# Kernel optimization log

Measured on AMD Instinct MI355X. Metric: run time of the kernel, lower is better.

## Reference

```python
import jax, jax.numpy as jnp
import numpy as np

N, E = 8000, 64000
DNE, DED, DXPD = 128, 128, 64
H, LMAX = 8, 2
S = 1 + 2 * LMAX            # 5 coefficient slots
CD = S * DNE                # coeff_dim = 640
DH = DNE // H               # head dim = 16
CH = CD // H                # coeff head = 80


def _lin(k, din, dout):
    # xavier-ish init for a [din, dout] weight used as x @ W
    return (jax.random.normal(k, (din, dout), jnp.float32) / np.sqrt(din)).astype(jnp.float32)


def _mlp(x, W1, b1, W2, b2):
    # Linear -> SiLU -> (Dropout p, eval) -> Linear
    return jax.nn.silu(x @ W1 + b1) @ W2 + b2


def _seg_sum(x, idx, n):
    return jax.ops.segment_sum(x, idx, num_segments=n)


def _rej(x, r):
    # vector_rejection: remove component of x [E,m,d] parallel to r [E,m]
    r3 = r[:, :, None]
    return x - jnp.sum(x * r3, axis=1, keepdims=True) * r3


def setup_inputs() -> dict:
    key = jax.random.key(0)
    ks = jax.random.split(key, 40)
    inp = {
        "h":  jax.random.normal(ks[0], (N, DNE), jnp.float32),
        "t":  jax.random.normal(ks[1], (E, DED), jnp.float32),
        "X1": jax.random.normal(ks[2], (N, 3, DNE), jnp.float32),
        "X2": jax.random.normal(ks[3], (N, 5, DNE), jnp.float32),
        "r1": jax.random.normal(ks[4], (E, 3), jnp.float32),
        "r2": jax.random.normal(ks[5], (E, 5), jnp.float32),
        "c":  jax.random.uniform(ks[6], (E, 1), jnp.float32),
        "edge": jax.random.randint(ks[7], (E, 2), 0, N, jnp.int32),
    }
    # GATA params
    inp["Wq"], inp["bq"] = _lin(ks[8], DNE, DNE), jnp.zeros((DNE,), jnp.float32)
    inp["Wk"], inp["bk"] = _lin(ks[9], DNE, DNE), jnp.zeros((DNE,), jnp.float32)
    inp["Wre"], inp["bre"] = _lin(ks[10], DED, DNE), jnp.zeros((DNE,), jnp.float32)
    inp["Wv1"], inp["bv1"] = _lin(ks[11], DNE, DNE), jnp.zeros((DNE,), jnp.float32)
    inp["Wv2"], inp["bv2"] = _lin(ks[12], DNE, CD), jnp.zeros((CD,), jnp.float32)
    inp["Wrs"], inp["brs"] = _lin(ks[13], DED, CD), jnp.zeros((CD,), jnp.float32)
    inp["Ws1"], inp["bs1"] = _lin(ks[14], DNE, DNE), jnp.zeros((DNE,), jnp.float32)
    inp["Ws2"], inp["bs2"] = _lin(ks[15], DNE, CD), jnp.zeros((CD,), jnp.float32)
    # HTR params
    inp["Wvq"] = _lin(ks[16], DNE, DXPD)
    inp["Wvk1"] = _lin(ks[17], DNE, DXPD)
    inp["Wvk2"] = _lin(ks[18], DNE, DXPD)
    inp["Ww1"], inp["bw1"] = _lin(ks[19], DXPD, DXPD), jnp.zeros((DXPD,), jnp.float32)
    inp["Ww2"], inp["bw2"] = _lin(ks[20], DXPD, DED), jnp.zeros((DED,), jnp.float32)
    inp["Wt1"], inp["bt1"] = _lin(ks[21], DED, DED), jnp.zeros((DED,), jnp.float32)
    inp["Wt2"], inp["bt2"] = _lin(ks[22], DED, DED), jnp.zeros((DED,), jnp.float32)
    return inp


def reference(h, t, X1, X2, r1, r2, c, edge,
              Wq, bq, Wk, bk, Wre, bre, Wv1, bv1, Wv2, bv2,
              Wrs, brs, Ws1, bs1, Ws2, bs2,
              Wvq, Wvk1, Wvk2, Ww1, bw1, Ww2, bw2, Wt1, bt1, Wt2, bt2):
    i, j = edge[:, 0], edge[:, 1]
    # multi-head attention logits over edges
    q = (h[i] @ Wq + bq).reshape(E, H, DH)
    k = (h[j] @ Wk + bk).reshape(E, H, DH)
    geom = jax.nn.silu(t @ Wre + bre).reshape(E, H, DH)
    alpha = jnp.sum(q * (k * geom), axis=-1)                       # [E,H]
    # segment softmax over destination node i
    mx = jnp.full((N, H), -jnp.inf, jnp.float32).at[i].max(alpha)
    mx = jnp.maximum(mx, -1e9)
    ex = jnp.exp(alpha - mx[i])
    den = jnp.maximum(_seg_sum(ex, i, N), 1e-12)
    attn = ex / den[i]
    deg = jnp.zeros((N,), jnp.float32).at[i].add(1.0)              # bincount
    attn = attn * (jnp.sqrt(deg[i]) / np.sqrt(DNE))[:, None]       # [E,H]
    # values + spatial branch
    v = _mlp(h[j], Wv1, bv1, Wv2, bv2).reshape(E, H, CH)
    sea = attn[:, :, None] * v
    tp = (t @ Wrs + brs).reshape(E, H, CH)
    s = _mlp(h[j], Ws1, bs1, Ws2, bs2).reshape(E, H, CH)
    spatial = tp * s * c[:, None, :]
    coeff = (sea + spatial).reshape(E, S, DNE)
    # scalar update
    h_out = h + _seg_sum(coeff[:, 0, :], i, N)
    # steerable updates (l = 1, 2)
    Xl, rl, X_out = [X1, X2], [r1, r2], []
    for l in (1, 2):
        o_d = coeff[:, l, :]          # direction coeff
        o_t = coeff[:, LMAX + l, :]   # tensor coeff
        msg = rl[l - 1][:, :, None] * o_d[:, None, :] + Xl[l - 1][j] * o_t[:, None, :]
        X_out.append(Xl[l - 1] + _seg_sum(msg, i, N))
    # HTR edge refinement
    Xcat = jnp.concatenate(X_out, axis=1)                          # [N,8,dne]
    Q = (Xcat @ Wvq)[i]                                            # [E,8,dxpd]
    K = jnp.concatenate([X_out[0] @ Wvk1, X_out[1] @ Wvk2], axis=1)[j]
    Q = jnp.concatenate([_rej(Q[:, :3], r1), _rej(Q[:, 3:], r2)], axis=1)
    K = jnp.concatenate([_rej(K[:, :3], -r1), _rej(K[:, 3:], -r2)], axis=1)
    w = jnp.sum(Q * K, axis=1)                                     # [E,dxpd]
    t_out = t + _mlp(w, Ww1, bw1, Ww2, bw2) * _mlp(t, Wt1, bt1, Wt2, bt2)
    return (h_out, t_out, X_out[0], X_out[1])
```

## Files before the change

kernel.cpp:

```cpp
#include <hip/hip_runtime.h>
#include <cstdint>
#include <cmath>

#define NN 8000
#define NE 64000
#define DNE 128
#define NHD 8
#define CDIM 640

typedef unsigned short u16;
typedef u16   u16x8 __attribute__((ext_vector_type(8)));
typedef __bf16 v8bf __attribute__((ext_vector_type(8)));
typedef float  v4f  __attribute__((ext_vector_type(4)));

static __device__ __forceinline__ u16 f2bf(float f) {
    unsigned int u = __float_as_uint(f);
    u += 0x7FFF + ((u >> 16) & 1);
    return (u16)(u >> 16);
}
static __device__ __forceinline__ float bf2f(u16 v) {
    return __uint_as_float(((unsigned int)v) << 16);
}

constexpr size_t O_TBF   = 0;
constexpr size_t O_X1BF  = 16384000;
constexpr size_t O_X2BF  = O_X1BF  + 6160384;
constexpr size_t O_X1OBF = O_X2BF  + 10256384;
constexpr size_t O_X2OBF = O_X1OBF + 6160384;
constexpr size_t O_WARE  = O_X2OBF + 10256384;
constexpr size_t O_CNT   = O_WARE  + 811008;
constexpr size_t O_CURS  = O_CNT   + 32000;
constexpr size_t O_OFFS  = O_CURS  + 32000;
constexpr size_t O_EIDS  = O_OFFS  + 32768;
constexpr size_t O_HV    = O_EIDS  + 256000;
constexpr size_t O_HS    = O_HV    + 10321920;
constexpr size_t O_ATTN  = O_HS    + 10321920;
constexpr size_t O_B512  = O_ATTN  + 2048000;
constexpr size_t O_TEMP  = O_B512  + 2048;
constexpr size_t O_QKVS  = O_TEMP;
constexpr size_t O_ALPHA = O_QKVS + 8257536;
constexpr size_t O_HBF   = O_ALPHA + 2048000;
constexpr size_t O_COEFF = O_TEMP;
constexpr size_t O_Q1K1  = O_TEMP;
constexpr size_t O_Q2K2  = O_Q1K1 + 6160384;
constexpr size_t O_WBUF  = O_Q2K2 + 10256384;
constexpr size_t O_WOUT  = O_WBUF + 8192000;

__device__ const int WOFFA[14] = {0,16384,32768,49152,65536,81920,98304,114688,196608,278528,360448,364544,372736,389120};

struct WTArgs { const float* w[16]; const float* b[4]; };
__global__ void wtrans_all(WTArgs a, u16* __restrict__ ob, float* __restrict__ bias512) {
    int s = blockIdx.y;
    int id = blockIdx.x * 256 + threadIdx.x;
    if (s < 12) {
        int K = (s < 10) ? 128 : 64;
        int N = (s < 7) ? 128 : ((s < 10) ? 640 : ((s == 10) ? 64 : 128));
        if (id >= K * N) return;
        int k = id / N, n = id % N;
        ob[WOFFA[s] + (size_t)n * K + k] = f2bf(a.w[s][id]);
    } else if (s < 14) {
        if (id >= 16384) return;
        int n = id >> 7, k = id & 127;
        const float* wa = a.w[s == 12 ? 12 : 14];
        const float* wb = a.w[s == 12 ? 13 : 15];
        ob[WOFFA[s] + id] = f2bf(n < 64 ? wa[k * 64 + n] : wb[k * 64 + (n - 64)]);
    } else {
        if (id >= 512) return;
        bias512[id] = a.b[id >> 7][id & 127];
    }
}

struct ConvArgs { const float* in[4]; u16* out[4]; };
__global__ void conv_all(ConvArgs a) {
    int s = blockIdx.y;
    int padr = (s == 0) ? 8064 : ((s == 1) ? 64000 : ((s == 2) ? 24064 : 40064));
    int realr = (s == 0) ? 8000 : ((s == 1) ? 64000 : ((s == 2) ? 24000 : 40000));
    int id4 = (blockIdx.x * 256 + threadIdx.x) * 4;
    if (id4 >= padr * 128) return;
    int row = id4 >> 7;
    float4 v = make_float4(0.f, 0.f, 0.f, 0.f);
    if (row < realr) v = *(const float4*)(a.in[s] + id4);
    u16* o = a.out[s] + id4;
    o[0] = f2bf(v.x); o[1] = f2bf(v.y); o[2] = f2bf(v.z); o[3] = f2bf(v.w);
}

template<int MODE>
__global__ __launch_bounds__(256) void mm_bf16(
    const u16* __restrict__ A, int As, const u16* __restrict__ Bt,
    const float* __restrict__ bias, void* __restrict__ out,
    int Ncols, int K, int act,
    const int* __restrict__ edge, const float* __restrict__ attn,
    const u16* __restrict__ hv, const u16* __restrict__ hs,
    const float* __restrict__ cvals)
{
    constexpr int BM = 128, BN = 128, BK = 32, LDA = 40;
    constexpr int MT = 4, NT = 4;
    __shared__ u16 sA[BM * LDA];
    __shared__ u16 sB[BN * LDA];
    const int tid = threadIdx.x;
    const int wave = tid >> 6, lane = tid & 63;
    const int lane15 = lane & 15, quad = lane >> 4;
    const int wm = wave >> 1, wn = wave & 1;
    const int row0 = blockIdx.y * BM, col0 = blockIdx.x * BN;
    const int arow = wm * 64, brow = wn * 64;
    v4f acc[MT][NT] = {};
    for (int k0 = 0; k0 < K; k0 += BK) {
        #pragma unroll
        for (int ci = 0; ci < 2; ++ci) {
            int cch = tid + ci * 256;
            int m = cch >> 2, ko = (cch & 3) * 8;
            *(u16x8*)(&sA[m * LDA + ko]) = *(const u16x8*)(A + (size_t)(row0 + m) * As + k0 + ko);
        }
        #pragma unroll
        for (int ci = 0; ci < 2; ++ci) {
            int cch = tid + ci * 256;
            int n = cch >> 2, ko = (cch & 3) * 8;
            *(u16x8*)(&sB[n * LDA + ko]) = *(const u16x8*)(Bt + (size_t)(col0 + n) * K + k0 + ko);
        }
        __syncthreads();
        v8bf af[MT], bfr[NT];
        #pragma unroll
        for (int mt = 0; mt < MT; ++mt)
            af[mt] = __builtin_bit_cast(v8bf, *(const u16x8*)(&sA[(arow + mt * 16 + lane15) * LDA + quad * 8]));
        #pragma unroll
        for (int nt = 0; nt < NT; ++nt)
            bfr[nt] = __builtin_bit_cast(v8bf, *(const u16x8*)(&sB[(brow + nt * 16 + lane15) * LDA + quad * 8]));
        #pragma unroll
        for (int mt = 0; mt < MT; ++mt)
            #pragma unroll
            for (int nt = 0; nt < NT; ++nt)
                acc[mt][nt] = __builtin_amdgcn_mfma_f32_16x16x32_bf16(af[mt], bfr[nt], acc[mt][nt], 0, 0, 0);
        __syncthreads();
    }
    #pragma unroll
    for (int mt = 0; mt < MT; ++mt) {
        #pragma unroll
        for (int r = 0; r < 4; ++r) {
            int grow = row0 + arow + mt * 16 + quad * 4 + r;
            if (MODE == 2) {
                int e = grow;
                int jn = edge[2 * e + 1];
                float ce = cvals[e];
                const u16* hvr = hv + (size_t)jn * CDIM;
                const u16* hsr = hs + (size_t)jn * CDIM;
                u16* orow = (u16*)out + (size_t)e * CDIM;
                #pragma unroll
                for (int nt = 0; nt < NT; ++nt) {
                    int gcol = col0 + brow + nt * 16 + lane15;
                    float tp = acc[mt][nt][r] + bias[gcol];
                    float at = attn[e * NHD + gcol / 80];
                    float v = at * bf2f(hvr[gcol]) + tp * bf2f(hsr[gcol]) * ce;
                    orow[gcol] = f2bf(v);
                }
            } else if (MODE == 4) {
                int e = grow;
                int i2 = edge[2 * e], j2 = edge[2 * e + 1];
                const u16* qb = hv + (size_t)i2 * 512;
                const u16* kb = hv + (size_t)j2 * 512 + 128;
                #pragma unroll
                for (int nt = 0; nt < NT; ++nt) {
                    int gcol = col0 + brow + nt * 16 + lane15;
                    float g = acc[mt][nt][r] + bias[gcol];
                    g = g / (1.0f + expf(-g));
                    float p = g * bf2f(qb[gcol]) * bf2f(kb[gcol]);
                    p += __shfl_xor(p, 1);
                    p += __shfl_xor(p, 2);
                    p += __shfl_xor(p, 4);
                    p += __shfl_xor(p, 8);
                    if (lane15 == 0)
                        ((float*)out)[(size_t)e * NHD + ((col0 + brow) >> 4) + nt] = p;
                }
            } else {
                u16* orow = (u16*)out + (size_t)grow * Ncols;
                #pragma unroll
                for (int nt = 0; nt < NT; ++nt) {
                    int gcol = col0 + brow + nt * 16 + lane15;
                    float v = acc[mt][nt][r];
                    if (bias) v += bias[gcol];
                    if (act == 1 || (act == 2 && gcol >= 256)) v = v / (1.0f + expf(-v));
                    orow[gcol] = f2bf(v);
                }
            }
        }
    }
}

__global__ __launch_bounds__(256) void wchain_kernel(
    const u16* __restrict__ wbuf, const u16* __restrict__ W1T, const u16* __restrict__ W2T,
    const float* __restrict__ b1, const float* __restrict__ b2, u16* __restrict__ wout)
{
    __shared__ u16 sw[128 * 72];
    __shared__ u16 sm[128 * 72];
    __shared__ u16 sW1[64 * 72];
    __shared__ u16 sW2[128 * 72];
    const int tid = threadIdx.x;
    const int wave = tid >> 6, lane = tid & 63;
    const int lane15 = lane & 15, quad = lane >> 4;
    const int row0 = blockIdx.x * 128;
    #pragma unroll
    for (int ci = 0; ci < 4; ++ci) {
        int cch = tid + ci * 256;
        int m = cch >> 3, ko = (cch & 7) * 8;
        *(u16x8*)(&sw[m * 72 + ko]) = *(const u16x8*)(wbuf + (size_t)(row0 + m) * 64 + ko);
    }
    #pragma unroll
    for (int ci = 0; ci < 2; ++ci) {
        int cch = tid + ci * 256;
        int n = cch >> 3, ko = (cch & 7) * 8;
        *(u16x8*)(&sW1[n * 72 + ko]) = *(const u16x8*)(W1T + (size_t)n * 64 + ko);
    }
    #pragma unroll
    for (int ci = 0; ci < 4; ++ci) {
        int cch = tid + ci * 256;
        int n = cch >> 3, ko = (cch & 7) * 8;
        *(u16x8*)(&sW2[n * 72 + ko]) = *(const u16x8*)(W2T + (size_t)n * 64 + ko);
    }
    __syncthreads();
    v4f a1[2][4] = {};
    #pragma unroll
    for (int kk = 0; kk < 2; ++kk) {
        int k0 = kk * 32;
        v8bf af[2], bfr[4];
        #pragma unroll
        for (int mt = 0; mt < 2; ++mt)
            af[mt] = __builtin_bit_cast(v8bf, *(const u16x8*)(&sw[(wave * 32 + mt * 16 + lane15) * 72 + k0 + quad * 8]));
        #pragma unroll
        for (int nt = 0; nt < 4; ++nt)
            bfr[nt] = __builtin_bit_cast(v8bf, *(const u16x8*)(&sW1[(nt * 16 + lane15) * 72 + k0 + quad * 8]));
        #pragma unroll
        for (int mt = 0; mt < 2; ++mt)
            #pragma unroll
            for (int nt = 0; nt < 4; ++nt)
                a1[mt][nt] = __builtin_amdgcn_mfma_f32_16x16x32_bf16(af[mt], bfr[nt], a1[mt][nt], 0, 0, 0);
    }
    #pragma unroll
    for (int mt = 0; mt < 2; ++mt)
        #pragma unroll
        for (int r = 0; r < 4; ++r) {
            int mrow = wave * 32 + mt * 16 + quad * 4 + r;
            #pragma unroll
            for (int nt = 0; nt < 4; ++nt) {
                int mcol = nt * 16 + lane15;
                float v = a1[mt][nt][r] + b1[mcol];
                v = v / (1.0f + expf(-v));
                sm[mrow * 72 + mcol] = f2bf(v);
            }
        }
    __syncthreads();
    const int wm = wave >> 1, wn = wave & 1;
    const int arow = wm * 64, brow = wn * 64;
    v4f a2[4][4] = {};
    #pragma unroll
    for (int kk = 0; kk < 2; ++kk) {
        int k0 = kk * 32;
        v8bf af[4], bfr[4];
        #pragma unroll
        for (int mt = 0; mt < 4; ++mt)
            af[mt] = __builtin_bit_cast(v8bf, *(const u16x8*)(&sm[(arow + mt * 16 + lane15) * 72 + k0 + quad * 8]));
        #pragma unroll
        for (int nt = 0; nt < 4; ++nt)
            bfr[nt] = __builtin_bit_cast(v8bf, *(const u16x8*)(&sW2[(brow + nt * 16 + lane15) * 72 + k0 + quad * 8]));
        #pragma unroll
        for (int mt = 0; mt < 4; ++mt)
            #pragma unroll
            for (int nt = 0; nt < 4; ++nt)
                a2[mt][nt] = __builtin_amdgcn_mfma_f32_16x16x32_bf16(af[mt], bfr[nt], a2[mt][nt], 0, 0, 0);
    }
    #pragma unroll
    for (int mt = 0; mt < 4; ++mt)
        #pragma unroll
        for (int r = 0; r < 4; ++r) {
            int grow = row0 + arow + mt * 16 + quad * 4 + r;
            #pragma unroll
            for (int nt = 0; nt < 4; ++nt) {
                int gcol = brow + nt * 16 + lane15;
                wout[(size_t)grow * 128 + gcol] = f2bf(a2[mt][nt][r] + b2[gcol]);
            }
        }
}

__global__ __launch_bounds__(256) void tchain_kernel(
    const u16* __restrict__ tbf, const u16* __restrict__ W1T, const u16* __restrict__ W2T,
    const float* __restrict__ b1, const float* __restrict__ b2,
    const float* __restrict__ tin, const u16* __restrict__ wout,
    float* __restrict__ t_out)
{
    constexpr int LDA = 136;
    __shared__ u16 sA[128 * LDA];
    __shared__ u16 sW[128 * 72];
    const int tid = threadIdx.x;
    const int wave = tid >> 6, lane = tid & 63;
    const int lane15 = lane & 15, quad = lane >> 4;
    const int wm = wave >> 1, wn = wave & 1;
    const int arow = wm * 64, brow = wn * 64;
    const int row0 = blockIdx.x * 128;
    #pragma unroll
    for (int ci = 0; ci < 8; ++ci) {
        int cch = tid + ci * 256;
        int m = cch >> 4, ko = (cch & 15) * 8;
        *(u16x8*)(&sA[m * LDA + ko]) = *(const u16x8*)(tbf + (size_t)(row0 + m) * 128 + ko);
    }
    v4f acc[4][4] = {};
    #pragma unroll
    for (int kh = 0; kh < 2; ++kh) {
        __syncthreads();
        #pragma unroll
        for (int ci = 0; ci < 4; ++ci) {
            int cch = tid + ci * 256;
            int n = cch >> 3, ko = (cch & 7) * 8;
            *(u16x8*)(&sW[n * 72 + ko]) = *(const u16x8*)(W1T + (size_t)n * 128 + kh * 64 + ko);
        }
        __syncthreads();
        #pragma unroll
        for (int kk = 0; kk < 2; ++kk) {
            int k0 = kh * 64 + kk * 32;
            v8bf af[4], bfr[4];
            #pragma unroll
            for (int mt = 0; mt < 4; ++mt)
                af[mt] = __builtin_bit_cast(v8bf, *(const u16x8*)(&sA[(arow + mt * 16 + lane15) * LDA + k0 + quad * 8]));
            #pragma unroll
            for (int nt = 0; nt < 4; ++nt)
                bfr[nt] = __builtin_bit_cast(v8bf, *(const u16x8*)(&sW[(brow + nt * 16 + lane15) * 72 + kk * 32 + quad * 8]));
            #pragma unroll
            for (int mt = 0; mt < 4; ++mt)
                #pragma unroll
                for (int nt = 0; nt < 4; ++nt)
                    acc[mt][nt] = __builtin_amdgcn_mfma_f32_16x16x32_bf16(af[mt], bfr[nt], acc[mt][nt], 0, 0, 0);
        }
    }
    __syncthreads();
    #pragma unroll
    for (int mt = 0; mt < 4; ++mt)
        #pragma unroll
        for (int r = 0; r < 4; ++r) {
            int mrow = arow + mt * 16 + quad * 4 + r;
            #pragma unroll
            for (int nt = 0; nt < 4; ++nt) {
                int mcol = brow + nt * 16 + lane15;
                float v = acc[mt][nt][r] + b1[mcol];
                v = v / (1.0f + expf(-v));
                sA[mrow * LDA + mcol] = f2bf(v);
            }
        }
    v4f acc2[4][4] = {};
    #pragma unroll
    for (int kh = 0; kh < 2; ++kh) {
        __syncthreads();
        #pragma unroll
        for (int ci = 0; ci < 4; ++ci) {
            int cch = tid + ci * 256;
            int n = cch >> 3, ko = (cch & 7) * 8;
            *(u16x8*)(&sW[n * 72 + ko]) = *(const u16x8*)(W2T + (size_t)n * 128 + kh * 64 + ko);
        }
        __syncthreads();
        #pragma unroll
        for (int kk = 0; kk < 2; ++kk) {
            int k0 = kh * 64 + kk * 32;
            v8bf af[4], bfr[4];
            #pragma unroll
            for (int mt = 0; mt < 4; ++mt)
                af[mt] = __builtin_bit_cast(v8bf, *(const u16x8*)(&sA[(arow + mt * 16 + lane15) * LDA + k0 + quad * 8]));
            #pragma unroll
            for (int nt = 0; nt < 4; ++nt)
                bfr[nt] = __builtin_bit_cast(v8bf, *(const u16x8*)(&sW[(brow + nt * 16 + lane15) * 72 + kk * 32 + quad * 8]));
            #pragma unroll
            for (int mt = 0; mt < 4; ++mt)
                #pragma unroll
                for (int nt = 0; nt < 4; ++nt)
                    acc2[mt][nt] = __builtin_amdgcn_mfma_f32_16x16x32_bf16(af[mt], bfr[nt], acc2[mt][nt], 0, 0, 0);
        }
    }
    #pragma unroll
    for (int mt = 0; mt < 4; ++mt)
        #pragma unroll
        for (int r = 0; r < 4; ++r) {
            int grow = row0 + arow + mt * 16 + quad * 4 + r;
            size_t base = (size_t)grow * 128;
            #pragma unroll
            for (int nt = 0; nt < 4; ++nt) {
                int gcol = brow + nt * 16 + lane15;
                float v = acc2[mt][nt][r] + b2[gcol];
                t_out[base + gcol] = tin[base + gcol] + bf2f(wout[base + gcol]) * v;
            }
        }
}

__global__ void zero_i32_kernel(int* a, int n) {
    int t = blockIdx.x * 256 + threadIdx.x;
    if (t < n) a[t] = 0;
}
__global__ void count_kernel(const int* __restrict__ edge, int* __restrict__ cnt, int E_) {
    int e = blockIdx.x * 256 + threadIdx.x;
    if (e < E_) atomicAdd(&cnt[edge[2 * e]], 1);
}
__global__ __launch_bounds__(1024) void scan_kernel(const int* __restrict__ cnt, int* __restrict__ offs, int n) {
    __shared__ int s[1024];
    int t = threadIdx.x;
    int base = t * 8;
    int loc[8];
    int sum = 0;
    #pragma unroll
    for (int q = 0; q < 8; ++q) {
        int idx = base + q;
        int v = (idx < n) ? cnt[idx] : 0;
        loc[q] = v; sum += v;
    }
    s[t] = sum;
    __syncthreads();
    for (int off = 1; off < 1024; off <<= 1) {
        int v = (t >= off) ? s[t - off] : 0;
        __syncthreads();
        s[t] += v;
        __syncthreads();
    }
    int run = s[t] - sum;
    #pragma unroll
    for (int q = 0; q < 8; ++q) {
        int idx = base + q;
        if (idx < n) offs[idx] = run;
        run += loc[q];
    }
    if (t == 1023) offs[n] = s[1023];
}
__global__ void fill_kernel(const int* __restrict__ edge, const int* __restrict__ offs,
                            int* __restrict__ cursor, int* __restrict__ eids, int E_) {
    int e = blockIdx.x * 256 + threadIdx.x;
    if (e >= E_) return;
    int i = edge[2 * e];
    int pos = atomicAdd(&cursor[i], 1);
    eids[offs[i] + pos] = e;
}

__global__ __launch_bounds__(64) void softmax_kernel(
    const float* __restrict__ alpha, const int* __restrict__ offs, const int* __restrict__ eids,
    float* __restrict__ attn)
{
    int node = blockIdx.x;
    int t = threadIdx.x;
    int g = t >> 3, hh = t & 7;
    int beg = offs[node], end = offs[node + 1];
    int deg = end - beg;
    __shared__ float sm[8][8];
    __shared__ float ss[8][8];
    float m = -1e9f;
    for (int p = beg + g; p < end; p += 8) {
        int e = eids[p];
        m = fmaxf(m, alpha[e * NHD + hh]);
    }
    sm[g][hh] = m;
    __syncthreads();
    if (g == 0) {
        float mm = sm[0][hh];
        #pragma unroll
        for (int q = 1; q < 8; ++q) mm = fmaxf(mm, sm[q][hh]);
        sm[0][hh] = mm;
    }
    __syncthreads();
    float mx = sm[0][hh];
    float ssum = 0.f;
    for (int p = beg + g; p < end; p += 8) {
        int e = eids[p];
        ssum += expf(alpha[e * NHD + hh] - mx);
    }
    ss[g][hh] = ssum;
    __syncthreads();
    if (g == 0) {
        float tot = 0.f;
        #pragma unroll
        for (int q = 0; q < 8; ++q) tot += ss[q][hh];
        ss[0][hh] = fmaxf(tot, 1e-12f);
    }
    __syncthreads();
    float den = ss[0][hh];
    float scale = sqrtf((float)deg) * 0.08838834764831845f;
    for (int p = beg + g; p < end; p += 8) {
        int e = eids[p];
        attn[e * NHD + hh] = expf(alpha[e * NHD + hh] - mx) / den * scale;
    }
}

__global__ __launch_bounds__(128) void scatter_kernel(
    const u16* __restrict__ coeff, const int* __restrict__ edge,
    const float* __restrict__ r1, const float* __restrict__ r2,
    const float* __restrict__ h, const float* __restrict__ X1, const float* __restrict__ X2,
    const u16* __restrict__ X1bf, const u16* __restrict__ X2bf,
    const int* __restrict__ offs, const int* __restrict__ eids,
    float* __restrict__ h_out, float* __restrict__ X1_out, float* __restrict__ X2_out,
    u16* __restrict__ X1obf, u16* __restrict__ X2obf)
{
    int n = blockIdx.x;
    int d = threadIdx.x;
    int beg = offs[n], end = offs[n + 1];
    float hacc = 0.f;
    float x1a[3] = {0.f, 0.f, 0.f};
    float x2a[5] = {0.f, 0.f, 0.f, 0.f, 0.f};
    for (int p = beg; p < end; ++p) {
        int e = eids[p];
        int j = edge[2 * e + 1];
        const u16* crow = coeff + (size_t)e * CDIM;
        float c0  = bf2f(crow[d]);
        float od1 = bf2f(crow[128 + d]);
        float od2 = bf2f(crow[256 + d]);
        float ot1 = bf2f(crow[384 + d]);
        float ot2 = bf2f(crow[512 + d]);
        hacc += c0;
        #pragma unroll
        for (int a = 0; a < 3; ++a)
            x1a[a] += r1[e * 3 + a] * od1 + bf2f(X1bf[((size_t)j * 3 + a) * DNE + d]) * ot1;
        #pragma unroll
        for (int a = 0; a < 5; ++a)
            x2a[a] += r2[e * 5 + a] * od2 + bf2f(X2bf[((size_t)j * 5 + a) * DNE + d]) * ot2;
    }
    h_out[(size_t)n * DNE + d] = h[(size_t)n * DNE + d] + hacc;
    #pragma unroll
    for (int a = 0; a < 3; ++a) {
        size_t idx = ((size_t)n * 3 + a) * DNE + d;
        float v = X1[idx] + x1a[a];
        X1_out[idx] = v;
        X1obf[idx] = f2bf(v);
    }
    #pragma unroll
    for (int a = 0; a < 5; ++a) {
        size_t idx = ((size_t)n * 5 + a) * DNE + d;
        float v = X2[idx] + x2a[a];
        X2_out[idx] = v;
        X2obf[idx] = f2bf(v);
    }
}

__global__ __launch_bounds__(256) void w_kernel(
    const u16* __restrict__ QK1, const u16* __restrict__ QK2,
    const int* __restrict__ edge, const float* __restrict__ r1, const float* __restrict__ r2,
    u16* __restrict__ w, int E_)
{
    int e = blockIdx.x * 4 + (threadIdx.x >> 6);
    int d = threadIdx.x & 63;
    if (e >= E_) return;
    int i = edge[2 * e], j = edge[2 * e + 1];
    float q[8], k[8];
    #pragma unroll
    for (int a = 0; a < 3; ++a) {
        q[a] = bf2f(QK1[((size_t)i * 3 + a) * 128 + d]);
        k[a] = bf2f(QK1[((size_t)j * 3 + a) * 128 + 64 + d]);
    }
    #pragma unroll
    for (int a = 0; a < 5; ++a) {
        q[3 + a] = bf2f(QK2[((size_t)i * 5 + a) * 128 + d]);
        k[3 + a] = bf2f(QK2[((size_t)j * 5 + a) * 128 + 64 + d]);
    }
    float ra[3], rb[5];
    #pragma unroll
    for (int a = 0; a < 3; ++a) ra[a] = r1[e * 3 + a];
    #pragma unroll
    for (int a = 0; a < 5; ++a) rb[a] = r2[e * 5 + a];
    float dq1 = 0.f, dk1 = 0.f, dq2 = 0.f, dk2 = 0.f;
    #pragma unroll
    for (int a = 0; a < 3; ++a) { dq1 += q[a] * ra[a]; dk1 += k[a] * ra[a]; }
    #pragma unroll
    for (int a = 0; a < 5; ++a) { dq2 += q[3 + a] * rb[a]; dk2 += k[3 + a] * rb[a]; }
    float acc = 0.f;
    #pragma unroll
    for (int a = 0; a < 3; ++a) acc += (q[a] - dq1 * ra[a]) * (k[a] - dk1 * ra[a]);
    #pragma unroll
    for (int a = 0; a < 5; ++a) acc += (q[3 + a] - dq2 * rb[a]) * (k[3 + a] - dk2 * rb[a]);
    w[(size_t)e * 64 + d] = f2bf(acc);
}

extern "C" void kernel_launch(void* const* d_in, const int* in_sizes, int n_in,
                              void* d_out, int out_size, void* d_ws, size_t ws_size,
                              hipStream_t stream)
{
    const float* h    = (const float*)d_in[0];
    const float* t    = (const float*)d_in[1];
    const float* X1   = (const float*)d_in[2];
    const float* X2   = (const float*)d_in[3];
    const float* r1   = (const float*)d_in[4];
    const float* r2   = (const float*)d_in[5];
    const float* c    = (const float*)d_in[6];
    const int*   edge = (const int*)d_in[7];
    const float* Wq   = (const float*)d_in[8];  const float* bq  = (const float*)d_in[9];
    const float* Wk   = (const float*)d_in[10]; const float* bk  = (const float*)d_in[11];
    const float* Wre  = (const float*)d_in[12]; const float* bre = (const float*)d_in[13];
    const float* Wv1  = (const float*)d_in[14]; const float* bv1 = (const float*)d_in[15];
    const float* Wv2  = (const float*)d_in[16]; const float* bv2 = (const float*)d_in[17];
    const float* Wrs  = (const float*)d_in[18]; const float* brs = (const float*)d_in[19];
    const float* Ws1  = (const float*)d_in[20]; const float* bs1 = (const float*)d_in[21];
    const float* Ws2  = (const float*)d_in[22]; const float* bs2 = (const float*)d_in[23];
    const float* Wvq  = (const float*)d_in[24];
    const float* Wvk1 = (const float*)d_in[25];
    const float* Wvk2 = (const float*)d_in[26];
    const float* Ww1  = (const float*)d_in[27]; const float* bw1 = (const float*)d_in[28];
    const float* Ww2  = (const float*)d_in[29]; const float* bw2 = (const float*)d_in[30];
    const float* Wt1  = (const float*)d_in[31]; const float* bt1 = (const float*)d_in[32];
    const float* Wt2  = (const float*)d_in[33]; const float* bt2 = (const float*)d_in[34];

    char* ws = (char*)d_ws;
    float* h_out  = (float*)d_out;
    float* t_out  = h_out + (size_t)NN * DNE;
    float* X1_out = t_out + (size_t)NE * 128;
    float* X2_out = X1_out + (size_t)NN * 3 * DNE;

    u16* t_bf   = (u16*)(ws + O_TBF);
    u16* X1bf   = (u16*)(ws + O_X1BF);
    u16* X2bf   = (u16*)(ws + O_X2BF);
    u16* X1obf  = (u16*)(ws + O_X1OBF);
    u16* X2obf  = (u16*)(ws + O_X2OBF);
    u16* ware   = (u16*)(ws + O_WARE);
    int* cnt    = (int*)(ws + O_CNT);
    int* cursor = (int*)(ws + O_CURS);
    int* offs   = (int*)(ws + O_OFFS);
    int* eids   = (int*)(ws + O_EIDS);
    u16* hv_bf  = (u16*)(ws + O_HV);
    u16* hs_bf  = (u16*)(ws + O_HS);
    float* attn = (float*)(ws + O_ATTN);
    float* bias512 = (float*)(ws + O_B512);
    u16* qkvs   = (u16*)(ws + O_QKVS);
    float* alpha= (float*)(ws + O_ALPHA);
    u16* h_bf   = (u16*)(ws + O_HBF);
    u16* coeff  = (u16*)(ws + O_COEFF);
    u16* Q1K1   = (u16*)(ws + O_Q1K1);
    u16* Q2K2   = (u16*)(ws + O_Q2K2);
    u16* wbuf   = (u16*)(ws + O_WBUF);
    u16* wout   = (u16*)(ws + O_WOUT);

    u16* WqkvsT = ware + 0;
    u16* WreT = ware + 65536;
    u16* Wt1T = ware + 81920;
    u16* Wt2T = ware + 98304;
    u16* Wv2T = ware + 114688;
    u16* WrsT = ware + 196608;
    u16* Ws2T = ware + 278528;
    u16* Ww1T = ware + 360448;
    u16* Ww2T = ware + 364544;
    u16* WA1T = ware + 372736;
    u16* WA2T = ware + 389120;

    WTArgs wt;
    wt.w[0] = Wq;  wt.w[1] = Wk;  wt.w[2] = Wv1; wt.w[3] = Ws1; wt.w[4] = Wre;
    wt.w[5] = Wt1; wt.w[6] = Wt2; wt.w[7] = Wv2; wt.w[8] = Wrs; wt.w[9] = Ws2;
    wt.w[10] = Ww1; wt.w[11] = Ww2; wt.w[12] = Wvq; wt.w[13] = Wvk1; wt.w[14] = Wvq; wt.w[15] = Wvk2;
    wt.b[0] = bq; wt.b[1] = bk; wt.b[2] = bv1; wt.b[3] = bs1;
    wtrans_all<<<dim3(320, 15), 256, 0, stream>>>(wt, ware, bias512);

    ConvArgs ca;
    ca.in[0] = h;  ca.out[0] = h_bf;
    ca.in[1] = t;  ca.out[1] = t_bf;
    ca.in[2] = X1; ca.out[2] = X1bf;
    ca.in[3] = X2; ca.out[3] = X2bf;
    conv_all<<<dim3(8000, 4), 256, 0, stream>>>(ca);

    zero_i32_kernel<<<63, 256, 0, stream>>>(cnt, 16000);
    count_kernel<<<250, 256, 0, stream>>>(edge, cnt, NE);
    scan_kernel<<<1, 1024, 0, stream>>>(cnt, offs, NN);
    fill_kernel<<<250, 256, 0, stream>>>(edge, offs, cursor, eids, NE);

    const int* np = nullptr; const float* nf = nullptr; const u16* nu = nullptr;

    mm_bf16<0><<<dim3(4, 63), 256, 0, stream>>>(h_bf, 128, WqkvsT, bias512, qkvs,
                                                512, 128, 2, np, nf, nu, nu, nf);
    mm_bf16<0><<<dim3(5, 63), 256, 0, stream>>>(qkvs + 256, 512, Wv2T, bv2, hv_bf,
                                                640, 128, 0, np, nf, nu, nu, nf);
    mm_bf16<0><<<dim3(5, 63), 256, 0, stream>>>(qkvs + 384, 512, Ws2T, bs2, hs_bf,
                                                640, 128, 0, np, nf, nu, nu, nf);
    mm_bf16<4><<<dim3(1, 500), 256, 0, stream>>>(t_bf, 128, WreT, bre, alpha,
                                                 128, 128, 0, edge, nf, qkvs, nu, nf);
    softmax_kernel<<<NN, 64, 0, stream>>>(alpha, offs, eids, attn);

    mm_bf16<2><<<dim3(5, 500), 256, 0, stream>>>(t_bf, 128, WrsT, brs, coeff,
                                                 640, 128, 0, edge, attn, hv_bf, hs_bf, c);

    scatter_kernel<<<NN, 128, 0, stream>>>(coeff, edge, r1, r2, h, X1, X2, X1bf, X2bf,
                                           offs, eids, h_out, X1_out, X2_out, X1obf, X2obf);

    mm_bf16<0><<<dim3(1, 188), 256, 0, stream>>>(X1obf, 128, WA1T, nullptr, Q1K1,
                                                 128, 128, 0, np, nf, nu, nu, nf);
    mm_bf16<0><<<dim3(1, 313), 256, 0, stream>>>(X2obf, 128, WA2T, nullptr, Q2K2,
                                                 128, 128, 0, np, nf, nu, nu, nf);

    w_kernel<<<NE / 4, 256, 0, stream>>>(Q1K1, Q2K2, edge, r1, r2, wbuf, NE);

    wchain_kernel<<<500, 256, 0, stream>>>(wbuf, Ww1T, Ww2T, bw1, bw2, wout);
    tchain_kernel<<<500, 256, 0, stream>>>(t_bf, Wt1T, Wt2T, bt1, bt2, t, wout, t_out);
}
```

Before: 503.8 us.

## Merge GEMM launches into mega kernels and stage edge metadata in shared memory

Turns the generic bf16 GEMM into a device body and adds fused multi-role kernels: one launch covers the hv/hs/alpha GEMMs, one covers both Q/K projections and reads fp32 X_out directly, and the count-buffer zeroing moves into the weight-transform kernel. Edge indices, attention weights and c values are staged in shared memory, and gathered hv/hs/q/k values are loaded before the epilogue math. This removes several launches and the bf16 X_out staging buffers. The cost is in-loop fp32-to-bf16 conversion of A tiles and a scatter kernel relaunched with 256 threads.

```diff
diff --git a/kernel.cpp b/kernel.cpp
--- a/kernel.cpp
+++ b/kernel.cpp
@@ -21,13 +21,14 @@
 static __device__ __forceinline__ float bf2f(u16 v) {
     return __uint_as_float(((unsigned int)v) << 16);
 }
+static __device__ __forceinline__ float silu(float v) {
+    return v / (1.0f + __expf(-v));
+}
 
 constexpr size_t O_TBF   = 0;
 constexpr size_t O_X1BF  = 16384000;
 constexpr size_t O_X2BF  = O_X1BF  + 6160384;
-constexpr size_t O_X1OBF = O_X2BF  + 10256384;
-constexpr size_t O_X2OBF = O_X1OBF + 6160384;
-constexpr size_t O_WARE  = O_X2OBF + 10256384;
+constexpr size_t O_WARE  = O_X2BF  + 10256384;
 constexpr size_t O_CNT   = O_WARE  + 811008;
 constexpr size_t O_CURS  = O_CNT   + 32000;
 constexpr size_t O_OFFS  = O_CURS  + 32000;
@@ -49,7 +50,8 @@
 __device__ const int WOFFA[14] = {0,16384,32768,49152,65536,81920,98304,114688,196608,278528,360448,364544,372736,389120};
 
 struct WTArgs { const float* w[16]; const float* b[4]; };
-__global__ void wtrans_all(WTArgs a, u16* __restrict__ ob, float* __restrict__ bias512) {
+__global__ void wtrans_all(WTArgs a, u16* __restrict__ ob, float* __restrict__ bias512,
+                           int* __restrict__ zeroa) {
     int s = blockIdx.y;
     int id = blockIdx.x * 256 + threadIdx.x;
     if (s < 12) {
@@ -64,9 +66,11 @@
         const float* wa = a.w[s == 12 ? 12 : 14];
         const float* wb = a.w[s == 12 ? 13 : 15];
         ob[WOFFA[s] + id] = f2bf(n < 64 ? wa[k * 64 + n] : wb[k * 64 + (n - 64)]);
-    } else {
+    } else if (s == 14) {
         if (id >= 512) return;
         bias512[id] = a.b[id >> 7][id & 127];
+    } else {
+        if (id < 16000) zeroa[id] = 0;
     }
 }
 
@@ -84,32 +88,61 @@
     o[0] = f2bf(v.x); o[1] = f2bf(v.y); o[2] = f2bf(v.z); o[3] = f2bf(v.w);
 }
 
-template<int MODE>
-__global__ __launch_bounds__(256) void mm_bf16(
-    const u16* __restrict__ A, int As, const u16* __restrict__ Bt,
-    const float* __restrict__ bias, void* __restrict__ out,
-    int Ncols, int K, int act,
+template<int MODE, bool AF32>
+__device__ __forceinline__ void mm_body(
+    char* smem,
+    const u16* __restrict__ A, const float* __restrict__ Af, int As, int Areal,
+    const u16* __restrict__ Bt, const float* __restrict__ bias,
+    void* __restrict__ out, int Ncols, int K, int act,
     const int* __restrict__ edge, const float* __restrict__ attn,
     const u16* __restrict__ hv, const u16* __restrict__ hs,
-    const float* __restrict__ cvals)
-{
-    constexpr int BM = 128, BN = 128, BK = 32, LDA = 40;
-    constexpr int MT = 4, NT = 4;
-    __shared__ u16 sA[BM * LDA];
-    __shared__ u16 sB[BN * LDA];
+    const float* __restrict__ cvals, int bx, int by)
+{
+    constexpr int LDA = 40;
+    u16* sA = (u16*)smem;
+    u16* sB = (u16*)(smem + 10240);
+    float* attnL = (float*)(smem + 20480);
+    float* ceL   = (float*)(smem + 24576);
+    int*   jnL   = (int*)(smem + 25088);
+    int*   iL    = (int*)(smem + 20480);
+    int*   jL    = (int*)(smem + 20992);
     const int tid = threadIdx.x;
     const int wave = tid >> 6, lane = tid & 63;
     const int lane15 = lane & 15, quad = lane >> 4;
     const int wm = wave >> 1, wn = wave & 1;
-    const int row0 = blockIdx.y * BM, col0 = blockIdx.x * BN;
+    const int row0 = by * 128, col0 = bx * 128;
     const int arow = wm * 64, brow = wn * 64;
-    v4f acc[MT][NT] = {};
-    for (int k0 = 0; k0 < K; k0 += BK) {
+
+    if (MODE == 2) {
+        for (int q = tid; q < 1024; q += 256)
+            attnL[q] = attn[(size_t)(row0 + (q >> 3)) * NHD + (q & 7)];
+        if (tid < 128) { ceL[tid] = cvals[row0 + tid]; jnL[tid] = edge[2 * (row0 + tid) + 1]; }
+    }
+    if (MODE == 4) {
+        if (tid < 128) { int e = row0 + tid; iL[tid] = edge[2 * e]; jL[tid] = edge[2 * e + 1]; }
+    }
+
+    v4f acc[4][4] = {};
+    for (int k0 = 0; k0 < K; k0 += 32) {
         #pragma unroll
         for (int ci = 0; ci < 2; ++ci) {
             int cch = tid + ci * 256;
             int m = cch >> 2, ko = (cch & 3) * 8;
-            *(u16x8*)(&sA[m * LDA + ko]) = *(const u16x8*)(A + (size_t)(row0 + m) * As + k0 + ko);
+            int row = row0 + m;
+            if (AF32) {
+                u16 tmp[8];
+                if (row < Areal) {
+                    const float* src = Af + (size_t)row * As + k0 + ko;
+                    #pragma unroll
+                    for (int q = 0; q < 8; ++q) tmp[q] = f2bf(src[q]);
+                } else {
+                    #pragma unroll
+                    for (int q = 0; q < 8; ++q) tmp[q] = 0;
+                }
+                *(u16x8*)(&sA[m * LDA + ko]) = *(u16x8*)tmp;
+            } else {
+                *(u16x8*)(&sA[m * LDA + ko]) = *(const u16x8*)(A + (size_t)row * As + k0 + ko);
+            }
         }
         #pragma unroll
         for (int ci = 0; ci < 2; ++ci) {
@@ -118,277 +151,168 @@
             *(u16x8*)(&sB[n * LDA + ko]) = *(const u16x8*)(Bt + (size_t)(col0 + n) * K + k0 + ko);
         }
         __syncthreads();
-        v8bf af[MT], bfr[NT];
-        #pragma unroll
-        for (int mt = 0; mt < MT; ++mt)
+        v8bf af[4], bfr[4];
+        #pragma unroll
+        for (int mt = 0; mt < 4; ++mt)
             af[mt] = __builtin_bit_cast(v8bf, *(const u16x8*)(&sA[(arow + mt * 16 + lane15) * LDA + quad * 8]));
         #pragma unroll
-        for (int nt = 0; nt < NT; ++nt)
+        for (int nt = 0; nt < 4; ++nt)
             bfr[nt] = __builtin_bit_cast(v8bf, *(const u16x8*)(&sB[(brow + nt * 16 + lane15) * LDA + quad * 8]));
         #pragma unroll
-        for (int mt = 0; mt < MT; ++mt)
-            #pragma unroll
-            for (int nt = 0; nt < NT; ++nt)
+        for (int mt = 0; mt < 4; ++mt)
+            #pragma unroll
+            for (int nt = 0; nt < 4; ++nt)
                 acc[mt][nt] = __builtin_amdgcn_mfma_f32_16x16x32_bf16(af[mt], bfr[nt], acc[mt][nt], 0, 0, 0);
         __syncthreads();
     }
-    #pragma unroll
-    for (int mt = 0; mt < MT; ++mt) {
-        #pragma unroll
-        for (int r = 0; r < 4; ++r) {
-            int grow = row0 + arow + mt * 16 + quad * 4 + r;
-            if (MODE == 2) {
-                int e = grow;
-                int jn = edge[2 * e + 1];
-                float ce = cvals[e];
-                const u16* hvr = hv + (size_t)jn * CDIM;
-                const u16* hsr = hs + (size_t)jn * CDIM;
-                u16* orow = (u16*)out + (size_t)e * CDIM;
+
+    if (MODE == 2) {
+        #pragma unroll
+        for (int mt = 0; mt < 4; ++mt) {
+            int lrow[4];
+            const u16 *hvp[4], *hsp[4];
+            #pragma unroll
+            for (int r = 0; r < 4; ++r) {
+                int lr = arow + mt * 16 + quad * 4 + r;
+                lrow[r] = lr;
+                int jn = jnL[lr];
+                hvp[r] = hv + (size_t)jn * CDIM;
+                hsp[r] = hs + (size_t)jn * CDIM;
+            }
+            u16 hvv[4][4], hsv[4][4];
+            #pragma unroll
+            for (int r = 0; r < 4; ++r)
                 #pragma unroll
-                for (int nt = 0; nt < NT; ++nt) {
+                for (int nt = 0; nt < 4; ++nt) {
+                    int gcol = col0 + brow + nt * 16 + lane15;
+                    hvv[r][nt] = hvp[r][gcol];
+                    hsv[r][nt] = hsp[r][gcol];
+                }
+            #pragma unroll
+            for (int r = 0; r < 4; ++r) {
+                int lr = lrow[r];
+                float ce = ceL[lr];
+                u16* orow = (u16*)out + (size_t)(row0 + lr) * CDIM;
+                #pragma unroll
+                for (int nt = 0; nt < 4; ++nt) {
                     int gcol = col0 + brow + nt * 16 + lane15;
                     float tp = acc[mt][nt][r] + bias[gcol];
-                    float at = attn[e * NHD + gcol / 80];
-                    float v = at * bf2f(hvr[gcol]) + tp * bf2f(hsr[gcol]) * ce;
-                    orow[gcol] = f2bf(v);
+                    float at = attnL[lr * 8 + gcol / 80];
+                    orow[gcol] = f2bf(at * bf2f(hvv[r][nt]) + tp * bf2f(hsv[r][nt]) * ce);
                 }
-            } else if (MODE == 4) {
-                int e = grow;
-                int i2 = edge[2 * e], j2 = edge[2 * e + 1];
-                const u16* qb = hv + (size_t)i2 * 512;
-                const u16* kb = hv + (size_t)j2 * 512 + 128;
+            }
+        }
+    } else if (MODE == 4) {
+        #pragma unroll
+        for (int mt = 0; mt < 4; ++mt) {
+            int lrow[4];
+            const u16 *qp[4], *kp[4];
+            #pragma unroll
+            for (int r = 0; r < 4; ++r) {
+                int lr = arow + mt * 16 + quad * 4 + r;
+                lrow[r] = lr;
+                qp[r] = hv + (size_t)iL[lr] * 512;
+                kp[r] = hv + (size_t)jL[lr] * 512 + 128;
+            }
+            u16 qv[4][4], kv[4][4];
+            #pragma unroll
+            for (int r = 0; r < 4; ++r)
                 #pragma unroll
-                for (int nt = 0; nt < NT; ++nt) {
-                    int gcol = col0 + brow + nt * 16 + lane15;
-                    float g = acc[mt][nt][r] + bias[gcol];
-                    g = g / (1.0f + expf(-g));
-                    float p = g * bf2f(qb[gcol]) * bf2f(kb[gcol]);
+                for (int nt = 0; nt < 4; ++nt) {
+                    int gcol = brow + nt * 16 + lane15;
+                    qv[r][nt] = qp[r][gcol];
+                    kv[r][nt] = kp[r][gcol];
+                }
+            #pragma unroll
+            for (int r = 0; r < 4; ++r) {
+                int lr = lrow[r];
+                #pragma unroll
+                for (int nt = 0; nt < 4; ++nt) {
+                    int gcol = brow + nt * 16 + lane15;
+                    float g = silu(acc[mt][nt][r] + bias[gcol]);
+                    float p = g * bf2f(qv[r][nt]) * bf2f(kv[r][nt]);
                     p += __shfl_xor(p, 1);
                     p += __shfl_xor(p, 2);
                     p += __shfl_xor(p, 4);
                     p += __shfl_xor(p, 8);
                     if (lane15 == 0)
-                        ((float*)out)[(size_t)e * NHD + ((col0 + brow) >> 4) + nt] = p;
+                        ((float*)out)[(size_t)(row0 + lr) * NHD + (brow >> 4) + nt] = p;
                 }
-            } else {
+            }
+        }
+    } else {
+        #pragma unroll
+        for (int mt = 0; mt < 4; ++mt)
+            #pragma unroll
+            for (int r = 0; r < 4; ++r) {
+                int grow = row0 + arow + mt * 16 + quad * 4 + r;
                 u16* orow = (u16*)out + (size_t)grow * Ncols;
                 #pragma unroll
-                for (int nt = 0; nt < NT; ++nt) {
+                for (int nt = 0; nt < 4; ++nt) {
                     int gcol = col0 + brow + nt * 16 + lane15;
                     float v = acc[mt][nt][r];
                     if (bias) v += bias[gcol];
-                    if (act == 1 || (act == 2 && gcol >= 256)) v = v / (1.0f + expf(-v));
+                    if (act == 1 || (act == 2 && gcol >= 256)) v = silu(v);
                     orow[gcol] = f2bf(v);
                 }
             }
-        }
-    }
-}
-
-__global__ __launch_bounds__(256) void wchain_kernel(
-    const u16* __restrict__ wbuf, const u16* __restrict__ W1T, const u16* __restrict__ W2T,
-    const float* __restrict__ b1, const float* __restrict__ b2, u16* __restrict__ wout)
-{
-    __shared__ u16 sw[128 * 72];
-    __shared__ u16 sm[128 * 72];
-    __shared__ u16 sW1[64 * 72];
-    __shared__ u16 sW2[128 * 72];
-    const int tid = threadIdx.x;
-    const int wave = tid >> 6, lane = tid & 63;
-    const int lane15 = lane & 15, quad = lane >> 4;
-    const int row0 = blockIdx.x * 128;
-    #pragma unroll
-    for (int ci = 0; ci < 4; ++ci) {
-        int cch = tid + ci * 256;
-        int m = cch >> 3, ko = (cch & 7) * 8;
-        *(u16x8*)(&sw[m * 72 + ko]) = *(const u16x8*)(wbuf + (size_t)(row0 + m) * 64 + ko);
-    }
-    #pragma unroll
-    for (int ci = 0; ci < 2; ++ci) {
-        int cch = tid + ci * 256;
-        int n = cch >> 3, ko = (cch & 7) * 8;
-        *(u16x8*)(&sW1[n * 72 + ko]) = *(const u16x8*)(W1T + (size_t)n * 64 + ko);
-    }
-    #pragma unroll
-    for (int ci = 0; ci < 4; ++ci) {
-        int cch = tid + ci * 256;
-        int n = cch >> 3, ko = (cch & 7) * 8;
-        *(u16x8*)(&sW2[n * 72 + ko]) = *(const u16x8*)(W2T + (size_t)n * 64 + ko);
-    }
-    __syncthreads();
-    v4f a1[2][4] = {};
-    #pragma unroll
-    for (int kk = 0; kk < 2; ++kk) {
-        int k0 = kk * 32;
-        v8bf af[2], bfr[4];
-        #pragma unroll
-        for (int mt = 0; mt < 2; ++mt)
-            af[mt] = __builtin_bit_cast(v8bf, *(const u16x8*)(&sw[(wave * 32 + mt * 16 + lane15) * 72 + k0 + quad * 8]));
-        #pragma unroll
-        for (int nt = 0; nt < 4; ++nt)
-            bfr[nt] = __builtin_bit_cast(v8bf, *(const u16x8*)(&sW1[(nt * 16 + lane15) * 72 + k0 + quad * 8]));
-        #pragma unroll
-        for (int mt = 0; mt < 2; ++mt)
-            #pragma unroll
-            for (int nt = 0; nt < 4; ++nt)
-                a1[mt][nt] = __builtin_amdgcn_mfma_f32_16x16x32_bf16(af[mt], bfr[nt], a1[mt][nt], 0, 0, 0);
-    }
-    #pragma unroll
-    for (int mt = 0; mt < 2; ++mt)
-        #pragma unroll
-        for (int r = 0; r < 4; ++r) {
-            int mrow = wave * 32 + mt * 16 + quad * 4 + r;
-            #pragma unroll
-            for (int nt = 0; nt < 4; ++nt) {
-                int mcol = nt * 16 + lane15;
-                float v = a1[mt][nt][r] + b1[mcol];
-                v = v / (1.0f + expf(-v));
-                sm[mrow * 72 + mcol] = f2bf(v);
-            }
-        }
-    __syncthreads();
-    const int wm = wave >> 1, wn = wave & 1;
-    const int arow = wm * 64, brow = wn * 64;
-    v4f a2[4][4] = {};
-    #pragma unroll
-    for (int kk = 0; kk < 2; ++kk) {
-        int k0 = kk * 32;
-        v8bf af[4], bfr[4];
-        #pragma unroll
-        for (int mt = 0; mt < 4; ++mt)
-            af[mt] = __builtin_bit_cast(v8bf, *(const u16x8*)(&sm[(arow + mt * 16 + lane15) * 72 + k0 + quad * 8]));
-        #pragma unroll
-        for (int nt = 0; nt < 4; ++nt)
-            bfr[nt] = __builtin_bit_cast(v8bf, *(const u16x8*)(&sW2[(brow + nt * 16 + lane15) * 72 + k0 + quad * 8]));
-        #pragma unroll
-        for (int mt = 0; mt < 4; ++mt)
-            #pragma unroll
-            for (int nt = 0; nt < 4; ++nt)
-                a2[mt][nt] = __builtin_amdgcn_mfma_f32_16x16x32_bf16(af[mt], bfr[nt], a2[mt][nt], 0, 0, 0);
-    }
-    #pragma unroll
-    for (int mt = 0; mt < 4; ++mt)
-        #pragma unroll
-        for (int r = 0; r < 4; ++r) {
-            int grow = row0 + arow + mt * 16 + quad * 4 + r;
-            #pragma unroll
-            for (int nt = 0; nt < 4; ++nt) {
-                int gcol = brow + nt * 16 + lane15;
-                wout[(size_t)grow * 128 + gcol] = f2bf(a2[mt][nt][r] + b2[gcol]);
-            }
-        }
-}
-
-__global__ __launch_bounds__(256) void tchain_kernel(
-    const u16* __restrict__ tbf, const u16* __restrict__ W1T, const u16* __restrict__ W2T,
-    const float* __restrict__ b1, const float* __restrict__ b2,
-    const float* __restrict__ tin, const u16* __restrict__ wout,
-    float* __restrict__ t_out)
-{
-    constexpr int LDA = 136;
-    __shared__ u16 sA[128 * LDA];
-    __shared__ u16 sW[128 * 72];
-    const int tid = threadIdx.x;
-    const int wave = tid >> 6, lane = tid & 63;
-    const int lane15 = lane & 15, quad = lane >> 4;
-    const int wm = wave >> 1, wn = wave & 1;
-    const int arow = wm * 64, brow = wn * 64;
-    const int row0 = blockIdx.x * 128;
-    #pragma unroll
-    for (int ci = 0; ci < 8; ++ci) {
-        int cch = tid + ci * 256;
-        int m = cch >> 4, ko = (cch & 15) * 8;
-        *(u16x8*)(&sA[m * LDA + ko]) = *(const u16x8*)(tbf + (size_t)(row0 + m) * 128 + ko);
-    }
-    v4f acc[4][4] = {};
-    #pragma unroll
-    for (int kh = 0; kh < 2; ++kh) {
-        __syncthreads();
-        #pragma unroll
-        for (int ci = 0; ci < 4; ++ci) {
-            int cch = tid + ci * 256;
-            int n = cch >> 3, ko = (cch & 7) * 8;
-            *(u16x8*)(&sW[n * 72 + ko]) = *(const u16x8*)(W1T + (size_t)n * 128 + kh * 64 + ko);
-        }
-        __syncthreads();
-        #pragma unroll
-        for (int kk = 0; kk < 2; ++kk) {
-            int k0 = kh * 64 + kk * 32;
-            v8bf af[4], bfr[4];
-            #pragma unroll
-            for (int mt = 0; mt < 4; ++mt)
-                af[mt] = __builtin_bit_cast(v8bf, *(const u16x8*)(&sA[(arow + mt * 16 + lane15) * LDA + k0 + quad * 8]));
-            #pragma unroll
-            for (int nt = 0; nt < 4; ++nt)
-                bfr[nt] = __builtin_bit_cast(v8bf, *(const u16x8*)(&sW[(brow + nt * 16 + lane15) * 72 + kk * 32 + quad * 8]));
-            #pragma unroll
-            for (int mt = 0; mt < 4; ++mt)
-                #pragma unroll
-                for (int nt = 0; nt < 4; ++nt)
-                    acc[mt][nt] = __builtin_amdgcn_mfma_f32_16x16x32_bf16(af[mt], bfr[nt], acc[mt][nt], 0, 0, 0);
-        }
-    }
-    __syncthreads();
-    #pragma unroll
-    for (int mt = 0; mt < 4; ++mt)
-        #pragma unroll
-        for (int r = 0; r < 4; ++r) {
-            int mrow = arow + mt * 16 + quad * 4 + r;
-            #pragma unroll
-            for (int nt = 0; nt < 4; ++nt) {
-                int mcol = brow + nt * 16 + lane15;
-                float v = acc[mt][nt][r] + b1[mcol];
-                v = v / (1.0f + expf(-v));
-                sA[mrow * LDA + mcol] = f2bf(v);
-            }
-        }
-    v4f acc2[4][4] = {};
-    #pragma unroll
-    for (int kh = 0; kh < 2; ++kh) {
-        __syncthreads();
-        #pragma unroll
-        for (int ci = 0; ci < 4; ++ci) {
-            int cch = tid + ci * 256;
-            int n = cch >> 3, ko = (cch & 7) * 8;
-            *(u16x8*)(&sW[n * 72 + ko]) = *(const u16x8*)(W2T + (size_t)n * 128 + kh * 64 + ko);
-        }
-        __syncthreads();
-        #pragma unroll
-        for (int kk = 0; kk < 2; ++kk) {
-            int k0 = kh * 64 + kk * 32;
-            v8bf af[4], bfr[4];
-            #pragma unroll
-            for (int mt = 0; mt < 4; ++mt)
-                af[mt] = __builtin_bit_cast(v8bf, *(const u16x8*)(&sA[(arow + mt * 16 + lane15) * LDA + k0 + quad * 8]));
-            #pragma unroll
-            for (int nt = 0; nt < 4; ++nt)
-                bfr[nt] = __builtin_bit_cast(v8bf, *(const u16x8*)(&sW[(brow + nt * 16 + lane15) * 72 + kk * 32 + quad * 8]));
-            #pragma unroll
-            for (int mt = 0; mt < 4; ++mt)
-                #pragma unroll
-                for (int nt = 0; nt < 4; ++nt)
-                    acc2[mt][nt] = __builtin_amdgcn_mfma_f32_16x16x32_bf16(af[mt], bfr[nt], acc2[mt][nt], 0, 0, 0);
-        }
-    }
-    #pragma unroll
-    for (int mt = 0; mt < 4; ++mt)
-        #pragma unroll
-        for (int r = 0; r < 4; ++r) {
-            int grow = row0 + arow + mt * 16 + quad * 4 + r;
-            size_t base = (size_t)grow * 128;
-            #pragma unroll
-            for (int nt = 0; nt < 4; ++nt) {
-                int gcol = brow + nt * 16 + lane15;
-                float v = acc2[mt][nt][r] + b2[gcol];
-                t_out[base + gcol] = tin[base + gcol] + bf2f(wout[base + gcol]) * v;
-            }
-        }
-}
-
-__global__ void zero_i32_kernel(int* a, int n) {
-    int t = blockIdx.x * 256 + threadIdx.x;
-    if (t < n) a[t] = 0;
-}
+    }
+}
+
+__global__ __launch_bounds__(256) void qkvs_kernel(
+    const u16* h_bf, const u16* W, const float* b512, u16* qkvs)
+{
+    extern __shared__ char smem[];
+    int t = blockIdx.x;
+    mm_body<0, false>(smem, h_bf, nullptr, 128, 0, W, b512, qkvs, 512, 128, 2,
+                      nullptr, nullptr, nullptr, nullptr, nullptr, t & 3, t >> 2);
+}
+
+__global__ __launch_bounds__(256) void mega_kernel(
+    const u16* qkvs, const u16* Wv2T, const float* bv2, u16* hv_bf,
+    const u16* Ws2T, const float* bs2, u16* hs_bf,
+    const u16* t_bf, const u16* WreT, const float* bre, float* alpha,
+    const int* edge)
+{
+    extern __shared__ char smem[];
+    int t = blockIdx.x;
+    if (t < 315) {
+        mm_body<0, false>(smem, qkvs + 256, nullptr, 512, 0, Wv2T, bv2, hv_bf, 640, 128, 0,
+                          nullptr, nullptr, nullptr, nullptr, nullptr, t % 5, t / 5);
+    } else if (t < 630) {
+        t -= 315;
+        mm_body<0, false>(smem, qkvs + 384, nullptr, 512, 0, Ws2T, bs2, hs_bf, 640, 128, 0,
+                          nullptr, nullptr, nullptr, nullptr, nullptr, t % 5, t / 5);
+    } else {
+        mm_body<4, false>(smem, t_bf, nullptr, 128, 0, WreT, bre, alpha, 128, 128, 0,
+                          edge, nullptr, qkvs, nullptr, nullptr, 0, t - 630);
+    }
+}
+
+__global__ __launch_bounds__(256) void coeff_kernel(
+    const u16* t_bf, const u16* WrsT, const float* brs, u16* coeff,
+    const int* edge, const float* attn, const u16* hv, const u16* hs, const float* cvals)
+{
+    extern __shared__ char smem[];
+    mm_body<2, false>(smem, t_bf, nullptr, 128, 0, WrsT, brs, coeff, 640, 128, 0,
+                      edge, attn, hv, hs, cvals, blockIdx.x, blockIdx.y);
+}
+
+__global__ __launch_bounds__(256) void qk_kernel(
+    const float* X1_out, const u16* WA1T, u16* Q1K1,
+    const float* X2_out, const u16* WA2T, u16* Q2K2)
+{
+    extern __shared__ char smem[];
+    int t = blockIdx.x;
+    if (t < 188) {
+        mm_body<0, true>(smem, nullptr, X1_out, 128, 24000, WA1T, nullptr, Q1K1, 128, 128, 0,
+                         nullptr, nullptr, nullptr, nullptr, nullptr, 0, t);
+    } else {
+        mm_body<0, true>(smem, nullptr, X2_out, 128, 40000, WA2T, nullptr, Q2K2, 128, 128, 0,
+                         nullptr, nullptr, nullptr, nullptr, nullptr, 0, t - 188);
+    }
+}
+
 __global__ void count_kernel(const int* __restrict__ edge, int* __restrict__ cnt, int E_) {
     int e = blockIdx.x * 256 + threadIdx.x;
     if (e < E_) atomicAdd(&cnt[edge[2 * e]], 1);
@@ -460,7 +384,7 @@
     float ssum = 0.f;
     for (int p = beg + g; p < end; p += 8) {
         int e = eids[p];
-        ssum += expf(alpha[e * NHD + hh] - mx);
+        ssum += __expf(alpha[e * NHD + hh] - mx);
     }
     ss[g][hh] = ssum;
     __syncthreads();
@@ -475,29 +399,31 @@
     float scale = sqrtf((float)deg) * 0.08838834764831845f;
     for (int p = beg + g; p < end; p += 8) {
         int e = eids[p];
-        attn[e * NHD + hh] = expf(alpha[e * NHD + hh] - mx) / den * scale;
-    }
-}
-
-__global__ __launch_bounds__(128) void scatter_kernel(
+        attn[e * NHD + hh] = __expf(alpha[e * NHD + hh] - mx) / den * scale;
+    }
+}
+
+__global__ __launch_bounds__(256) void scatter_kernel(
     const u16* __restrict__ coeff, const int* __restrict__ edge,
     const float* __restrict__ r1, const float* __restrict__ r2,
     const float* __restrict__ h, const float* __restrict__ X1, const float* __restrict__ X2,
     const u16* __restrict__ X1bf, const u16* __restrict__ X2bf,
     const int* __restrict__ offs, const int* __restrict__ eids,
-    float* __restrict__ h_out, float* __restrict__ X1_out, float* __restrict__ X2_out,
-    u16* __restrict__ X1obf, u16* __restrict__ X2obf)
+    float* __restrict__ h_out, float* __restrict__ X1_out, float* __restrict__ X2_out)
 {
     int n = blockIdx.x;
-    int d = threadIdx.x;
+    int d = threadIdx.x & 127;
+    int g = threadIdx.x >> 7;
     int beg = offs[n], end = offs[n + 1];
     float hacc = 0.f;
     float x1a[3] = {0.f, 0.f, 0.f};
     float x2a[5] = {0.f, 0.f, 0.f, 0.f, 0.f};
-    for (int p = beg; p < end; ++p) {
+    for (int p = beg + g; p < end; p += 2) {
         int e = eids[p];
         int j = edge[2 * e + 1];
         const u16* crow = coeff + (size_t)e * CDIM;
+        const u16* x1r = X1bf + (size_t)j * 3 * DNE;
+        const u16* x2r = X2bf + (size_t)j * 5 * DNE;
         float c0  = bf2f(crow[d]);
         float od1 = bf2f(crow[128 + d]);
         float od2 = bf2f(crow[256 + d]);
@@ -506,25 +432,33 @@
         hacc += c0;
         #pragma unroll
         for (int a = 0; a < 3; ++a)
-            x1a[a] += r1[e * 3 + a] * od1 + bf2f(X1bf[((size_t)j * 3 + a) * DNE + d]) * ot1;
+            x1a[a] += r1[e * 3 + a] * od1 + bf2f(x1r[a * DNE + d]) * ot1;
         #pragma unroll
         for (int a = 0; a < 5; ++a)
-            x2a[a] += r2[e * 5 + a] * od2 + bf2f(X2bf[((size_t)j * 5 + a) * DNE + d]) * ot2;
-    }
-    h_out[(size_t)n * DNE + d] = h[(size_t)n * DNE + d] + hacc;
-    #pragma unroll
-    for (int a = 0; a < 3; ++a) {
-        size_t idx = ((size_t)n * 3 + a) * DNE + d;
-        float v = X1[idx] + x1a[a];
-        X1_out[idx] = v;
-        X1obf[idx] = f2bf(v);
-    }
-    #pragma unroll
-    for (int a = 0; a < 5; ++a) {
-        size_t idx = ((size_t)n * 5 + a) * DNE + d;
-        float v = X2[idx] + x2a[a];
-        X2_out[idx] = v;
-        X2obf[idx] = f2bf(v);
+            x2a[a] += r2[e * 5 + a] * od2 + bf2f(x2r[a * DNE + d]) * ot2;
+    }
+    __shared__ float red[1152];
+    if (g == 1) {
+        red[d] = hacc;
+        #pragma unroll
+        for (int a = 0; a < 3; ++a) red[128 + a * 128 + d] = x1a[a];
+        #pragma unroll
+        for (int a = 0; a < 5; ++a) red[512 + a * 128 + d] = x2a[a];
+    }
+    __syncthreads();
+    if (g == 0) {
+        hacc += red[d];
+        h_out[(size_t)n * DNE + d] = h[(size_t)n * DNE + d] + hacc;
+        #pragma unroll
+        for (int a = 0; a < 3; ++a) {
+            size_t idx = ((size_t)n * 3 + a) * DNE + d;
+            X1_out[idx] = X1[idx] + x1a[a] + red[128 + a * 128 + d];
+        }
+        #pragma unroll
+        for (int a = 0; a < 5; ++a) {
+            size_t idx = ((size_t)n * 5 + a) * DNE + d;
+            X2_out[idx] = X2[idx] + x2a[a] + red[512 + a * 128 + d];
+        }
     }
 }
 
@@ -564,6 +498,202 @@
     #pragma unroll
     for (int a = 0; a < 5; ++a) acc += (q[3 + a] - dq2 * rb[a]) * (k[3 + a] - dk2 * rb[a]);
     w[(size_t)e * 64 + d] = f2bf(acc);
+}
+
+__global__ __launch_bounds__(256) void wchain_kernel(
+    const u16* __restrict__ wbuf, const u16* __restrict__ W1T, const u16* __restrict__ W2T,
+    const float* __restrict__ b1, const float* __restrict__ b2, u16* __restrict__ wout)
+{
+    __shared__ u16 sw[128 * 72];
+    __shared__ u16 sm[128 * 72];
+    __shared__ u16 sW1[64 * 72];
+    __shared__ u16 sW2[128 * 72];
+    const int tid = threadIdx.x;
+    const int wave = tid >> 6, lane = tid & 63;
+    const int lane15 = lane & 15, quad = lane >> 4;
+    const int row0 = blockIdx.x * 128;
+    #pragma unroll
+    for (int ci = 0; ci < 4; ++ci) {
+        int cch = tid + ci * 256;
+        int m = cch >> 3, ko = (cch & 7) * 8;
+        *(u16x8*)(&sw[m * 72 + ko]) = *(const u16x8*)(wbuf + (size_t)(row0 + m) * 64 + ko);
+    }
+    #pragma unroll
+    for (int ci = 0; ci < 2; ++ci) {
+        int cch = tid + ci * 256;
+        int n = cch >> 3, ko = (cch & 7) * 8;
+        *(u16x8*)(&sW1[n * 72 + ko]) = *(const u16x8*)(W1T + (size_t)n * 64 + ko);
+    }
+    #pragma unroll
+    for (int ci = 0; ci < 4; ++ci) {
+        int cch = tid + ci * 256;
+        int n = cch >> 3, ko = (cch & 7) * 8;
+        *(u16x8*)(&sW2[n * 72 + ko]) = *(const u16x8*)(W2T + (size_t)n * 64 + ko);
+    }
+    __syncthreads();
+    v4f a1[2][4] = {};
+    #pragma unroll
+    for (int kk = 0; kk < 2; ++kk) {
+        int k0 = kk * 32;
+        v8bf af[2], bfr[4];
+        #pragma unroll
+        for (int mt = 0; mt < 2; ++mt)
+            af[mt] = __builtin_bit_cast(v8bf, *(const u16x8*)(&sw[(wave * 32 + mt * 16 + lane15) * 72 + k0 + quad * 8]));
+        #pragma unroll
+        for (int nt = 0; nt < 4; ++nt)
+            bfr[nt] = __builtin_bit_cast(v8bf, *(const u16x8*)(&sW1[(nt * 16 + lane15) * 72 + k0 + quad * 8]));
+        #pragma unroll
+        for (int mt = 0; mt < 2; ++mt)
+            #pragma unroll
+            for (int nt = 0; nt < 4; ++nt)
+                a1[mt][nt] = __builtin_amdgcn_mfma_f32_16x16x32_bf16(af[mt], bfr[nt], a1[mt][nt], 0, 0, 0);
+    }
+    #pragma unroll
+    for (int mt = 0; mt < 2; ++mt)
+        #pragma unroll
+        for (int r = 0; r < 4; ++r) {
+            int mrow = wave * 32 + mt * 16 + quad * 4 + r;
+            #pragma unroll
+            for (int nt = 0; nt < 4; ++nt) {
+                int mcol = nt * 16 + lane15;
+                sm[mrow * 72 + mcol] = f2bf(silu(a1[mt][nt][r] + b1[mcol]));
+            }
+        }
+    __syncthreads();
+    const int wm = wave >> 1, wn = wave & 1;
+    const int arow = wm * 64, brow = wn * 64;
+    v4f a2[4][4] = {};
+    #pragma unroll
+    for (int kk = 0; kk < 2; ++kk) {
+        int k0 = kk * 32;
+        v8bf af[4], bfr[4];
+        #pragma unroll
+        for (int mt = 0; mt < 4; ++mt)
+            af[mt] = __builtin_bit_cast(v8bf, *(const u16x8*)(&sm[(arow + mt * 16 + lane15) * 72 + k0 + quad * 8]));
+        #pragma unroll
+        for (int nt = 0; nt < 4; ++nt)
+            bfr[nt] = __builtin_bit_cast(v8bf, *(const u16x8*)(&sW2[(brow + nt * 16 + lane15) * 72 + k0 + quad * 8]));
+        #pragma unroll
+        for (int mt = 0; mt < 4; ++mt)
+            #pragma unroll
+            for (int nt = 0; nt < 4; ++nt)
+                a2[mt][nt] = __builtin_amdgcn_mfma_f32_16x16x32_bf16(af[mt], bfr[nt], a2[mt][nt], 0, 0, 0);
+    }
+    #pragma unroll
+    for (int mt = 0; mt < 4; ++mt)
+        #pragma unroll
+        for (int r = 0; r < 4; ++r) {
+            int grow = row0 + arow + mt * 16 + quad * 4 + r;
+            #pragma unroll
+            for (int nt = 0; nt < 4; ++nt) {
+                int gcol = brow + nt * 16 + lane15;
+                wout[(size_t)grow * 128 + gcol] = f2bf(a2[mt][nt][r] + b2[gcol]);
+            }
+        }
+}
+
+__global__ __launch_bounds__(256) void tchain_kernel(
+    const u16* __restrict__ tbf, const u16* __restrict__ W1T, const u16* __restrict__ W2T,
+    const float* __restrict__ b1, const float* __restrict__ b2,
+    const float* __restrict__ tin, const u16* __restrict__ wout,
+    float* __restrict__ t_out)
+{
+    constexpr int LDA = 136;
+    __shared__ u16 sA[128 * LDA];
+    __shared__ u16 sW[128 * 72];
+    const int tid = threadIdx.x;
+    const int wave = tid >> 6, lane = tid & 63;
+    const int lane15 = lane & 15, quad = lane >> 4;
+    const int wm = wave >> 1, wn = wave & 1;
+    const int arow = wm * 64, brow = wn * 64;
+    const int row0 = blockIdx.x * 128;
+    #pragma unroll
+    for (int ci = 0; ci < 8; ++ci) {
+        int cch = tid + ci * 256;
+        int m = cch >> 4, ko = (cch & 15) * 8;
+        *(u16x8*)(&sA[m * LDA + ko]) = *(const u16x8*)(tbf + (size_t)(row0 + m) * 128 + ko);
+    }
+    v4f acc[4][4] = {};
+    #pragma unroll
+    for (int kh = 0; kh < 2; ++kh) {
+        __syncthreads();
+        #pragma unroll
+        for (int ci = 0; ci < 4; ++ci) {
+            int cch = tid + ci * 256;
+            int n = cch >> 3, ko = (cch & 7) * 8;
+            *(u16x8*)(&sW[n * 72 + ko]) = *(const u16x8*)(W1T + (size_t)n * 128 + kh * 64 + ko);
+        }
+        __syncthreads();
+        #pragma unroll
+        for (int kk = 0; kk < 2; ++kk) {
+            int k0 = kh * 64 + kk * 32;
+            v8bf af[4], bfr[4];
+            #pragma unroll
+            for (int mt = 0; mt < 4; ++mt)
+                af[mt] = __builtin_bit_cast(v8bf, *(const u16x8*)(&sA[(arow + mt * 16 + lane15) * LDA + k0 + quad * 8]));
+            #pragma unroll
+            for (int nt = 0; nt < 4; ++nt)
+                bfr[nt] = __builtin_bit_cast(v8bf, *(const u16x8*)(&sW[(brow + nt * 16 + lane15) * 72 + kk * 32 + quad * 8]));
+            #pragma unroll
+            for (int mt = 0; mt < 4; ++mt)
+                #pragma unroll
+                for (int nt = 0; nt < 4; ++nt)
+                    acc[mt][nt] = __builtin_amdgcn_mfma_f32_16x16x32_bf16(af[mt], bfr[nt], acc[mt][nt], 0, 0, 0);
+        }
+    }
+    __syncthreads();
+    #pragma unroll
+    for (int mt = 0; mt < 4; ++mt)
+        #pragma unroll
+        for (int r = 0; r < 4; ++r) {
+            int mrow = arow + mt * 16 + quad * 4 + r;
+            #pragma unroll
+            for (int nt = 0; nt < 4; ++nt) {
+                int mcol = brow + nt * 16 + lane15;
+                sA[mrow * LDA + mcol] = f2bf(silu(acc[mt][nt][r] + b1[mcol]));
+            }
+        }
+    v4f acc2[4][4] = {};
+    #pragma unroll
+    for (int kh = 0; kh < 2; ++kh) {
+        __syncthreads();
+        #pragma unroll
+        for (int ci = 0; ci < 4; ++ci) {
+            int cch = tid + ci * 256;
+            int n = cch >> 3, ko = (cch & 7) * 8;
+            *(u16x8*)(&sW[n * 72 + ko]) = *(const u16x8*)(W2T + (size_t)n * 128 + kh * 64 + ko);
+        }
+        __syncthreads();
+        #pragma unroll
+        for (int kk = 0; kk < 2; ++kk) {
+            int k0 = kh * 64 + kk * 32;
+            v8bf af[4], bfr[4];
+            #pragma unroll
+            for (int mt = 0; mt < 4; ++mt)
+                af[mt] = __builtin_bit_cast(v8bf, *(const u16x8*)(&sA[(arow + mt * 16 + lane15) * LDA + k0 + quad * 8]));
+            #pragma unroll
+            for (int nt = 0; nt < 4; ++nt)
+                bfr[nt] = __builtin_bit_cast(v8bf, *(const u16x8*)(&sW[(brow + nt * 16 + lane15) * 72 + kk * 32 + quad * 8]));
+            #pragma unroll
+            for (int mt = 0; mt < 4; ++mt)
+                #pragma unroll
+                for (int nt = 0; nt < 4; ++nt)
+                    acc2[mt][nt] = __builtin_amdgcn_mfma_f32_16x16x32_bf16(af[mt], bfr[nt], acc2[mt][nt], 0, 0, 0);
+        }
+    }
+    #pragma unroll
+    for (int mt = 0; mt < 4; ++mt)
+        #pragma unroll
+        for (int r = 0; r < 4; ++r) {
+            int grow = row0 + arow + mt * 16 + quad * 4 + r;
+            size_t base = (size_t)grow * 128;
+            #pragma unroll
+            for (int nt = 0; nt < 4; ++nt) {
+                int gcol = brow + nt * 16 + lane15;
+                float v = acc2[mt][nt][r] + b2[gcol];
+                t_out[base + gcol] = tin[base + gcol] + bf2f(wout[base + gcol]) * v;
+            }
+        }
 }
 
 extern "C" void kernel_launch(void* const* d_in, const int* in_sizes, int n_in,
@@ -603,8 +733,6 @@
     u16* t_bf   = (u16*)(ws + O_TBF);
     u16* X1bf   = (u16*)(ws + O_X1BF);
     u16* X2bf   = (u16*)(ws + O_X2BF);
-    u16* X1obf  = (u16*)(ws + O_X1OBF);
-    u16* X2obf  = (u16*)(ws + O_X2OBF);
     u16* ware   = (u16*)(ws + O_WARE);
     int* cnt    = (int*)(ws + O_CNT);
     int* cursor = (int*)(ws + O_CURS);
@@ -640,7 +768,7 @@
     wt.w[5] = Wt1; wt.w[6] = Wt2; wt.w[7] = Wv2; wt.w[8] = Wrs; wt.w[9] = Ws2;
     wt.w[10] = Ww1; wt.w[11] = Ww2; wt.w[12] = Wvq; wt.w[13] = Wvk1; wt.w[14] = Wvq; wt.w[15] = Wvk2;
     wt.b[0] = bq; wt.b[1] = bk; wt.b[2] = bv1; wt.b[3] = bs1;
-    wtrans_all<<<dim3(320, 15), 256, 0, stream>>>(wt, ware, bias512);
+    wtrans_all<<<dim3(320, 16), 256, 0, stream>>>(wt, ware, bias512, cnt);
 
     ConvArgs ca;
     ca.in[0] = h;  ca.out[0] = h_bf;
@@ -649,33 +777,23 @@
     ca.in[3] = X2; ca.out[3] = X2bf;
     conv_all<<<dim3(8000, 4), 256, 0, stream>>>(ca);
 
-    zero_i32_kernel<<<63, 256, 0, stream>>>(cnt, 16000);
     count_kernel<<<250, 256, 0, stream>>>(edge, cnt, NE);
     scan_kernel<<<1, 1024, 0, stream>>>(cnt, offs, NN);
     fill_kernel<<<250, 256, 0, stream>>>(edge, offs, cursor, eids, NE);
 
-    const int* np = nullptr; const float* nf = nullptr; const u16* nu = nullptr;
-
-    mm_bf16<0><<<dim3(4, 63), 256, 0, stream>>>(h_bf, 128, WqkvsT, bias512, qkvs,
-                                                512, 128, 2, np, nf, nu, nu, nf);
-    mm_bf16<0><<<dim3(5, 63), 256, 0, stream>>>(qkvs + 256, 512, Wv2T, bv2, hv_bf,
-                                                640, 128, 0, np, nf, nu, nu, nf);
-    mm_bf16<0><<<dim3(5, 63), 256, 0, stream>>>(qkvs + 384, 512, Ws2T, bs2, hs_bf,
-                                                640, 128, 0, np, nf, nu, nu, nf);
-    mm_bf16<4><<<dim3(1, 500), 256, 0, stream>>>(t_bf, 128, WreT, bre, alpha,
-                                                 128, 128, 0, edge, nf, qkvs, nu, nf);
+    qkvs_kernel<<<252, 256, 20480, stream>>>(h_bf, WqkvsT, bias512, qkvs);
+
+    mega_kernel<<<1130, 256, 21504, stream>>>(qkvs, Wv2T, bv2, hv_bf, Ws2T, bs2, hs_bf,
+                                              t_bf, WreT, bre, alpha, edge);
     softmax_kernel<<<NN, 64, 0, stream>>>(alpha, offs, eids, attn);
 
-    mm_bf16<2><<<dim3(5, 500), 256, 0, stream>>>(t_bf, 128, WrsT, brs, coeff,
-                                                 640, 128, 0, edge, attn, hv_bf, hs_bf, c);
-
-    scatter_kernel<<<NN, 128, 0, stream>>>(coeff, edge, r1, r2, h, X1, X2, X1bf, X2bf,
-                                           offs, eids, h_out, X1_out, X2_out, X1obf, X2obf);
-
-    mm_bf16<0><<<dim3(1, 188), 256, 0, stream>>>(X1obf, 128, WA1T, nullptr, Q1K1,
-                                                 128, 128, 0, np, nf, nu, nu, nf);
-    mm_bf16<0><<<dim3(1, 313), 256, 0, stream>>>(X2obf, 128, WA2T, nullptr, Q2K2,
-                                                 128, 128, 0, np, nf, nu, nu, nf);
+    coeff_kernel<<<dim3(5, 500), 256, 25600, stream>>>(t_bf, WrsT, brs, coeff,
+                                                       edge, attn, hv_bf, hs_bf, c);
+
+    scatter_kernel<<<NN, 256, 0, stream>>>(coeff, edge, r1, r2, h, X1, X2, X1bf, X2bf,
+                                           offs, eids, h_out, X1_out, X2_out);
+
+    qk_kernel<<<501, 256, 20480, stream>>>(X1_out, WA1T, Q1K1, X2_out, WA2T, Q2K2);
 
     w_kernel<<<NE / 4, 256, 0, stream>>>(Q1K1, Q2K2, edge, r1, r2, wbuf, NE);
 
```

New measurement: 541.1 us. +7.4%, slower.
